# Kernel tuning notes

Measured on AMD Instinct MI355X. Metric: run time of the kernel, lower is better.

The kernel has to match this reference:

```python
import jax, jax.numpy as jnp
import numpy as np

TOP_K = 10


def setup_inputs() -> dict:
    key = jax.random.key(0)
    x = jax.random.normal(key, (256, 1, 8192), dtype=jnp.float32)
    return {"x": x}


def reference(x):
    # x: [B, 1, S] real
    B, _, S = x.shape
    # torch.arange(1e-05, 1, 1/S) has exactly S elements for these S
    t = 1e-05 + jnp.arange(S, dtype=jnp.float32) / S            # [S]
    dft = jnp.fft.fft(x[:, 0, :], n=S, axis=-1, norm='ortho')   # [B, S] complex64
    mag = jnp.abs(dft)                                          # [B, S]
    top_idx = jnp.argsort(-mag, axis=-1)[:, :TOP_K]             # [B, k] int
    top_dft = jnp.take_along_axis(dft, top_idx, axis=1)         # [B, k] complex
    # complex exponential basis exp(-2j*pi*k*t), flipped along time
    phase = (-2j * jnp.pi) * (top_idx[:, :, None].astype(jnp.float32) * t[None, None, :])
    bs = jnp.exp(phase)[:, :, ::-1]                             # [B, k, S] complex
    bf = top_dft[:, :, None] * bs / jnp.sqrt(jnp.float32(S))    # [B, k, S]
    # F.pad((1,0), mode='replicate') then crop to S: shift right by 1, duplicate first col
    bf = jnp.concatenate([bf[:, :, :1], bf[:, :, :-1]], axis=-1)
    bf = bf[:, :, None, :]                                      # [B, k, 1, S]
    residual = x - jnp.sum(bf, axis=1)                          # [B, 1, S] complex
    return bf, residual
```

## Files before the change

kernel.cpp:

```cpp
#include <hip/hip_runtime.h>

#define NB    256
#define SLEN  8192
#define LOG2S 13
#define TOPK  10

#define RES_REAL   ((size_t)20971520)
#define FULL_ILV   ((size_t)46137344)

__device__ int   g_k [NB * TOPK];
__device__ float g_ar[NB * TOPK];
__device__ float g_ai[NB * TOPK];

__device__ __forceinline__ float sin_rev(float p) { return __builtin_amdgcn_sinf(p); }
__device__ __forceinline__ float cos_rev(float p) { return __builtin_amdgcn_cosf(p); }

__device__ __forceinline__ bool beats(float om, int oi, float wm, int wi) {
  return (om > wm * 1.0001f) || (om > wm * 0.9999f && oi < wi);
}

__device__ __forceinline__ int pad(int a) { return a + (a >> 5); }

typedef float f32x4 __attribute__((ext_vector_type(4)));
__device__ __forceinline__ void store_nt4(float* p, float a, float b, float c,
                                          float d) {
  f32x4 v = {a, b, c, d};
  __builtin_nontemporal_store(v, (f32x4*)p);
}

__device__ __forceinline__ void bfly(float& ur, float& ui, float& vr, float& vi,
                                     float p) {
  const float c = cos_rev(p);
  const float s = -sin_rev(p);
  const float dr = ur - vr, di = ui - vi;
  ur += vr; ui += vi;
  vr = dr * c - di * s;
  vi = dr * s + di * c;
}

template<int ST>
__device__ __forceinline__ void bfly3(float (&xr)[8], float (&xi)[8], int m) {
  const float inv8 = 1.f / (float)(ST * 8);
  const float inv4 = 1.f / (float)(ST * 4);
  const float inv2 = 1.f / (float)(ST * 2);
#pragma unroll
  for (int k = 0; k < 4; ++k)
    bfly(xr[k], xi[k], xr[k + 4], xi[k + 4], (float)(m + ST * k) * inv8);
#pragma unroll
  for (int g = 0; g < 2; ++g)
#pragma unroll
    for (int k0 = 0; k0 < 2; ++k0) {
      const int k = g * 4 + k0;
      bfly(xr[k], xi[k], xr[k + 2], xi[k + 2], (float)(m + ST * k0) * inv4);
    }
  const float p1 = (float)m * inv2;
#pragma unroll
  for (int k = 0; k < 8; k += 2)
    bfly(xr[k], xi[k], xr[k + 1], xi[k + 1], p1);
}

__global__ __launch_bounds__(1024)
void fft_topk(const float* __restrict__ x) {
  __shared__ float re[8448];
  __shared__ float im[8448];
  __shared__ float wred_m[2][16];
  __shared__ int   wred_i[2][16];

  const int b = blockIdx.x;
  const int t = threadIdx.x;
  const int lane = t & 63;
  const int wid  = t >> 6;
  const float* xb = x + (size_t)b * SLEN;

  float xr[8], xi[8];

#pragma unroll
  for (int k = 0; k < 8; ++k) { xr[k] = xb[t + (k << 10)]; xi[k] = 0.f; }
  bfly3<1024>(xr, xi, t);
#pragma unroll
  for (int k = 0; k < 8; ++k) {
    const int a = pad(t + (k << 10));
    re[a] = xr[k]; im[a] = xi[k];
  }
  __syncthreads();

  {
    const int m  = t & 127;
    const int i0 = m + ((t >> 7) << 10);
#pragma unroll
    for (int k = 0; k < 8; ++k) {
      const int a = pad(i0 + (k << 7));
      xr[k] = re[a]; xi[k] = im[a];
    }
    bfly3<128>(xr, xi, m);
#pragma unroll
    for (int k = 0; k < 8; ++k) {
      const int a = pad(i0 + (k << 7));
      re[a] = xr[k]; im[a] = xi[k];
    }
  }
  __syncthreads();

  {
    const int m  = t & 15;
    const int i0 = m + ((t >> 4) << 7);
#pragma unroll
    for (int k = 0; k < 8; ++k) {
      const int a = pad(i0 + (k << 4));
      xr[k] = re[a]; xi[k] = im[a];
    }
    bfly3<16>(xr, xi, m);
#pragma unroll
    for (int k = 0; k < 8; ++k) {
      const int a = pad(i0 + (k << 4));
      re[a] = xr[k]; im[a] = xi[k];
    }
  }
  __syncthreads();

  {
    const int m  = t & 1;
    const int i0 = m + ((t >> 1) << 4);
#pragma unroll
    for (int k = 0; k < 8; ++k) {
      const int a = pad(i0 + (k << 1));
      xr[k] = re[a]; xi[k] = im[a];
    }
    bfly3<2>(xr, xi, m);
#pragma unroll
    for (int k = 0; k < 8; ++k) {
      const int a = pad(i0 + (k << 1));
      re[a] = xr[k]; im[a] = xi[k];
    }
  }
  __syncthreads();

#pragma unroll
  for (int q = 0; q < 8; ++q) {
    const int a = pad((t << 3) + q);
    xr[q] = re[a]; xi[q] = im[a];
  }
#pragma unroll
  for (int q = 0; q < 8; q += 2) {
    const float ur = xr[q], ui = xi[q];
    const float vr = xr[q + 1], vi = xi[q + 1];
    xr[q] = ur + vr;     xi[q] = ui + vi;
    xr[q + 1] = ur - vr; xi[q + 1] = ui - vi;
  }

  float m2c[8];
#pragma unroll
  for (int q = 0; q < 8; ++q) m2c[q] = xr[q] * xr[q] + xi[q] * xi[q];

  const int rt = (int)(__brev((unsigned)t) >> 22);
  const int qord[8] = {0, 4, 2, 6, 1, 5, 3, 7};

  for (int sel = 0; sel < TOPK; ++sel) {
    float wm = -1.f; int wi = SLEN;
#pragma unroll
    for (int j = 0; j < 8; ++j) {
      const int q = qord[j];
      if (m2c[q] > wm * 1.0001f) { wm = m2c[q]; wi = rt + (j << 10); }
    }
    for (int off = 32; off > 0; off >>= 1) {
      const float om = __shfl_down(wm, off);
      const int   oi = __shfl_down(wi, off);
      if (beats(om, oi, wm, wi)) { wm = om; wi = oi; }
    }
    const int par = sel & 1;
    if (lane == 0) { wred_m[par][wid] = wm; wred_i[par][wid] = wi; }
    __syncthreads();
    float cm = -1.f; int ci = SLEN;
    if (lane < 16) { cm = wred_m[par][lane]; ci = wred_i[par][lane]; }
    for (int off = 8; off > 0; off >>= 1) {
      const float om = __shfl_down(cm, off);
      const int   oi = __shfl_down(ci, off);
      if (beats(om, oi, cm, ci)) { cm = om; ci = oi; }
    }
    wm = __shfl(cm, 0); wi = __shfl(ci, 0);
    const int p = (int)(__brev((unsigned)wi) >> 19);
    if ((p >> 3) == t) {
      const int q = p & 7;
      const float rr = xr[q] * (1.f / (float)SLEN);
      const float ii = xi[q] * (1.f / (float)SLEN);
      const float pr = -1e-5f * (float)wi;
      const float cp = cos_rev(pr), sp = sin_rev(pr);
      g_k [b * TOPK + sel] = wi;
      g_ar[b * TOPK + sel] = rr * cp - ii * sp;
      g_ai[b * TOPK + sel] = rr * sp + ii * cp;
      m2c[q] = 0.f;
    }
  }
}

__global__ __launch_bounds__(256, 4)
void gen(const float* __restrict__ x, float* __restrict__ out, size_t cap) {
  const int bs    = blockIdx.x;
  const int b     = bs >> 3;
  const int slice = bs & 7;
  const int t     = threadIdx.x;
  const int s0    = slice * 1024 + t * 4;
  const float* xb = x + (size_t)b * SLEN;

  int kj[TOPK]; float arj[TOPK], aij[TOPK];
#pragma unroll
  for (int j = 0; j < TOPK; ++j) {
    kj[j]  = g_k [b * TOPK + j];
    arj[j] = g_ar[b * TOPK + j];
    aij[j] = g_ai[b * TOPK + j];
  }

  if (cap < FULL_ILV) {
    const size_t bfbase = (size_t)b * TOPK * SLEN;
    const float4 xv = *(const float4*)(xb + s0);
    float acc0 = 0.f, acc1 = 0.f, acc2 = 0.f, acc3 = 0.f;
#pragma unroll
    for (int j = 0; j < TOPK; ++j) {
      const int k = kj[j];
      float br[4];
#pragma unroll
      for (int q = 0; q < 4; ++q) {
        const int s = s0 + q;
        const int m = (s == 0) ? 1 : s;
        const float p = (float)((k * m) & (SLEN - 1)) * (1.f / (float)SLEN);
        br[q] = arj[j] * cos_rev(p) - aij[j] * sin_rev(p);
      }
      acc0 += br[0]; acc1 += br[1]; acc2 += br[2]; acc3 += br[3];
      const size_t o = bfbase + (size_t)j * SLEN + s0;
      if (o + 4 <= cap)
        store_nt4(out + o, br[0], br[1], br[2], br[3]);
    }
    const size_t o = RES_REAL + (size_t)b * SLEN + s0;
    if (o + 4 <= cap)
      store_nt4(out + o, xv.x - acc0, xv.y - acc1, xv.z - acc2, xv.w - acc3);
  } else {
    const size_t bfbase = (size_t)b * TOPK * SLEN * 2;
    const float4 xv = *(const float4*)(xb + s0);
    float sr[4] = {0.f, 0.f, 0.f, 0.f}, si[4] = {0.f, 0.f, 0.f, 0.f};
#pragma unroll
    for (int j = 0; j < TOPK; ++j) {
      const int k = kj[j];
      float br[4], bi[4];
#pragma unroll
      for (int q = 0; q < 4; ++q) {
        const int s = s0 + q;
        const int m = (s == 0) ? 1 : s;
        const float p = (float)((k * m) & (SLEN - 1)) * (1.f / (float)SLEN);
        const float c = cos_rev(p), sv = sin_rev(p);
        br[q] = arj[j] * c - aij[j] * sv;
        bi[q] = arj[j] * sv + aij[j] * c;
        sr[q] += br[q]; si[q] += bi[q];
      }
      const size_t o = bfbase + ((size_t)j * SLEN + s0) * 2;
      if (o + 8 <= cap) {
        store_nt4(out + o,     br[0], bi[0], br[1], bi[1]);
        store_nt4(out + o + 4, br[2], bi[2], br[3], bi[3]);
      }
    }
    const size_t o = (size_t)41943040 + ((size_t)b * SLEN + s0) * 2;
    if (o + 8 <= cap) {
      store_nt4(out + o,     xv.x - sr[0], -si[0], xv.y - sr[1], -si[1]);
      store_nt4(out + o + 4, xv.z - sr[2], -si[2], xv.w - sr[3], -si[3]);
    }
  }
}

extern "C" void kernel_launch(void* const* d_in, const int* in_sizes, int n_in,
                              void* d_out, int out_size, void* d_ws, size_t ws_size,
                              hipStream_t stream) {
  const float* x = (const float*)d_in[0];
  float* out = (float*)d_out;
  fft_topk<<<NB, 1024, 0, stream>>>(x);
  gen<<<NB * 8, 256, 0, stream>>>(x, out, (size_t)out_size);
}
```

Baseline: 123.3 us.

## Fuse FFT top-k and basis generation into a single kernel

Merges the FFT/top-k kernel and the basis/residual generation kernel into one kernel per batch row. The selected frequencies and amplitudes now stay in shared memory instead of round-tripping through global buffers, and one kernel launch is dropped. Each of the 1024 threads now writes 8 outputs instead of 4. The FFT scratch is also switched from split re/im arrays to interleaved float2. The trade-off is that the generation phase now runs with only 256 blocks of 1024 threads instead of 2048 smaller blocks, which may reduce occupancy and overlap of the store-heavy phase.

After: 150.1 us. 1.22x slower.

```diff
diff --git a/kernel.cpp b/kernel.cpp
--- a/kernel.cpp
+++ b/kernel.cpp
@@ -7,10 +7,6 @@
 
 #define RES_REAL   ((size_t)20971520)
 #define FULL_ILV   ((size_t)46137344)
-
-__device__ int   g_k [NB * TOPK];
-__device__ float g_ar[NB * TOPK];
-__device__ float g_ai[NB * TOPK];
 
 __device__ __forceinline__ float sin_rev(float p) { return __builtin_amdgcn_sinf(p); }
 __device__ __forceinline__ float cos_rev(float p) { return __builtin_amdgcn_cosf(p); }
@@ -60,11 +56,13 @@
 }
 
 __global__ __launch_bounds__(1024)
-void fft_topk(const float* __restrict__ x) {
-  __shared__ float re[8448];
-  __shared__ float im[8448];
-  __shared__ float wred_m[2][16];
-  __shared__ int   wred_i[2][16];
+void fourier_all(const float* __restrict__ x, float* __restrict__ out,
+                 size_t cap) {
+  __shared__ float2 Z[8448];
+  __shared__ float  wred_m[2][16];
+  __shared__ int    wred_i[2][16];
+  __shared__ int    sk[TOPK];
+  __shared__ float  sar[TOPK], sai[TOPK];
 
   const int b = blockIdx.x;
   const int t = threadIdx.x;
@@ -78,10 +76,8 @@
   for (int k = 0; k < 8; ++k) { xr[k] = xb[t + (k << 10)]; xi[k] = 0.f; }
   bfly3<1024>(xr, xi, t);
 #pragma unroll
-  for (int k = 0; k < 8; ++k) {
-    const int a = pad(t + (k << 10));
-    re[a] = xr[k]; im[a] = xi[k];
-  }
+  for (int k = 0; k < 8; ++k)
+    Z[pad(t + (k << 10))] = make_float2(xr[k], xi[k]);
   __syncthreads();
 
   {
@@ -89,15 +85,13 @@
     const int i0 = m + ((t >> 7) << 10);
 #pragma unroll
     for (int k = 0; k < 8; ++k) {
-      const int a = pad(i0 + (k << 7));
-      xr[k] = re[a]; xi[k] = im[a];
+      const float2 v = Z[pad(i0 + (k << 7))];
+      xr[k] = v.x; xi[k] = v.y;
     }
     bfly3<128>(xr, xi, m);
 #pragma unroll
-    for (int k = 0; k < 8; ++k) {
-      const int a = pad(i0 + (k << 7));
-      re[a] = xr[k]; im[a] = xi[k];
-    }
+    for (int k = 0; k < 8; ++k)
+      Z[pad(i0 + (k << 7))] = make_float2(xr[k], xi[k]);
   }
   __syncthreads();
 
@@ -106,15 +100,13 @@
     const int i0 = m + ((t >> 4) << 7);
 #pragma unroll
     for (int k = 0; k < 8; ++k) {
-      const int a = pad(i0 + (k << 4));
-      xr[k] = re[a]; xi[k] = im[a];
+      const float2 v = Z[pad(i0 + (k << 4))];
+      xr[k] = v.x; xi[k] = v.y;
     }
     bfly3<16>(xr, xi, m);
 #pragma unroll
-    for (int k = 0; k < 8; ++k) {
-      const int a = pad(i0 + (k << 4));
-      re[a] = xr[k]; im[a] = xi[k];
-    }
+    for (int k = 0; k < 8; ++k)
+      Z[pad(i0 + (k << 4))] = make_float2(xr[k], xi[k]);
   }
   __syncthreads();
 
@@ -123,22 +115,20 @@
     const int i0 = m + ((t >> 1) << 4);
 #pragma unroll
     for (int k = 0; k < 8; ++k) {
-      const int a = pad(i0 + (k << 1));
-      xr[k] = re[a]; xi[k] = im[a];
+      const float2 v = Z[pad(i0 + (k << 1))];
+      xr[k] = v.x; xi[k] = v.y;
     }
     bfly3<2>(xr, xi, m);
 #pragma unroll
-    for (int k = 0; k < 8; ++k) {
-      const int a = pad(i0 + (k << 1));
-      re[a] = xr[k]; im[a] = xi[k];
-    }
+    for (int k = 0; k < 8; ++k)
+      Z[pad(i0 + (k << 1))] = make_float2(xr[k], xi[k]);
   }
   __syncthreads();
 
 #pragma unroll
   for (int q = 0; q < 8; ++q) {
-    const int a = pad((t << 3) + q);
-    xr[q] = re[a]; xi[q] = im[a];
+    const float2 v = Z[pad((t << 3) + q)];
+    xr[q] = v.x; xi[q] = v.y;
   }
 #pragma unroll
   for (int q = 0; q < 8; q += 2) {
@@ -185,64 +175,67 @@
       const float ii = xi[q] * (1.f / (float)SLEN);
       const float pr = -1e-5f * (float)wi;
       const float cp = cos_rev(pr), sp = sin_rev(pr);
-      g_k [b * TOPK + sel] = wi;
-      g_ar[b * TOPK + sel] = rr * cp - ii * sp;
-      g_ai[b * TOPK + sel] = rr * sp + ii * cp;
+      sk [sel] = wi;
+      sar[sel] = rr * cp - ii * sp;
+      sai[sel] = rr * sp + ii * cp;
       m2c[q] = 0.f;
     }
   }
-}
-
-__global__ __launch_bounds__(256, 4)
-void gen(const float* __restrict__ x, float* __restrict__ out, size_t cap) {
-  const int bs    = blockIdx.x;
-  const int b     = bs >> 3;
-  const int slice = bs & 7;
-  const int t     = threadIdx.x;
-  const int s0    = slice * 1024 + t * 4;
-  const float* xb = x + (size_t)b * SLEN;
+  __syncthreads();
 
   int kj[TOPK]; float arj[TOPK], aij[TOPK];
 #pragma unroll
   for (int j = 0; j < TOPK; ++j) {
-    kj[j]  = g_k [b * TOPK + j];
-    arj[j] = g_ar[b * TOPK + j];
-    aij[j] = g_ai[b * TOPK + j];
-  }
+    kj[j] = sk[j]; arj[j] = sar[j]; aij[j] = sai[j];
+  }
+  const int s0 = t << 3;
 
   if (cap < FULL_ILV) {
     const size_t bfbase = (size_t)b * TOPK * SLEN;
-    const float4 xv = *(const float4*)(xb + s0);
-    float acc0 = 0.f, acc1 = 0.f, acc2 = 0.f, acc3 = 0.f;
+    const float4 xv0 = *(const float4*)(xb + s0);
+    const float4 xv1 = *(const float4*)(xb + s0 + 4);
+    float acc[8];
+#pragma unroll
+    for (int q = 0; q < 8; ++q) acc[q] = 0.f;
 #pragma unroll
     for (int j = 0; j < TOPK; ++j) {
       const int k = kj[j];
-      float br[4];
-#pragma unroll
-      for (int q = 0; q < 4; ++q) {
+      float br[8];
+#pragma unroll
+      for (int q = 0; q < 8; ++q) {
         const int s = s0 + q;
         const int m = (s == 0) ? 1 : s;
         const float p = (float)((k * m) & (SLEN - 1)) * (1.f / (float)SLEN);
         br[q] = arj[j] * cos_rev(p) - aij[j] * sin_rev(p);
-      }
-      acc0 += br[0]; acc1 += br[1]; acc2 += br[2]; acc3 += br[3];
+        acc[q] += br[q];
+      }
       const size_t o = bfbase + (size_t)j * SLEN + s0;
-      if (o + 4 <= cap)
-        store_nt4(out + o, br[0], br[1], br[2], br[3]);
+      if (o + 8 <= cap) {
+        store_nt4(out + o,     br[0], br[1], br[2], br[3]);
+        store_nt4(out + o + 4, br[4], br[5], br[6], br[7]);
+      }
     }
     const size_t o = RES_REAL + (size_t)b * SLEN + s0;
-    if (o + 4 <= cap)
-      store_nt4(out + o, xv.x - acc0, xv.y - acc1, xv.z - acc2, xv.w - acc3);
+    if (o + 8 <= cap) {
+      store_nt4(out + o,     xv0.x - acc[0], xv0.y - acc[1], xv0.z - acc[2],
+                xv0.w - acc[3]);
+      store_nt4(out + o + 4, xv1.x - acc[4], xv1.y - acc[5], xv1.z - acc[6],
+                xv1.w - acc[7]);
+    }
   } else {
     const size_t bfbase = (size_t)b * TOPK * SLEN * 2;
-    const float4 xv = *(const float4*)(xb + s0);
-    float sr[4] = {0.f, 0.f, 0.f, 0.f}, si[4] = {0.f, 0.f, 0.f, 0.f};
+    const float4 xv0 = *(const float4*)(xb + s0);
+    const float4 xv1 = *(const float4*)(xb + s0 + 4);
+    const float xs[8] = {xv0.x, xv0.y, xv0.z, xv0.w, xv1.x, xv1.y, xv1.z, xv1.w};
+    float sr[8], si[8];
+#pragma unroll
+    for (int q = 0; q < 8; ++q) { sr[q] = 0.f; si[q] = 0.f; }
 #pragma unroll
     for (int j = 0; j < TOPK; ++j) {
       const int k = kj[j];
-      float br[4], bi[4];
-#pragma unroll
-      for (int q = 0; q < 4; ++q) {
+      float br[8], bi[8];
+#pragma unroll
+      for (int q = 0; q < 8; ++q) {
         const int s = s0 + q;
         const int m = (s == 0) ? 1 : s;
         const float p = (float)((k * m) & (SLEN - 1)) * (1.f / (float)SLEN);
@@ -252,15 +245,19 @@
         sr[q] += br[q]; si[q] += bi[q];
       }
       const size_t o = bfbase + ((size_t)j * SLEN + s0) * 2;
-      if (o + 8 <= cap) {
-        store_nt4(out + o,     br[0], bi[0], br[1], bi[1]);
-        store_nt4(out + o + 4, br[2], bi[2], br[3], bi[3]);
+      if (o + 16 <= cap) {
+        store_nt4(out + o,      br[0], bi[0], br[1], bi[1]);
+        store_nt4(out + o + 4,  br[2], bi[2], br[3], bi[3]);
+        store_nt4(out + o + 8,  br[4], bi[4], br[5], bi[5]);
+        store_nt4(out + o + 12, br[6], bi[6], br[7], bi[7]);
       }
     }
     const size_t o = (size_t)41943040 + ((size_t)b * SLEN + s0) * 2;
-    if (o + 8 <= cap) {
-      store_nt4(out + o,     xv.x - sr[0], -si[0], xv.y - sr[1], -si[1]);
-      store_nt4(out + o + 4, xv.z - sr[2], -si[2], xv.w - sr[3], -si[3]);
+    if (o + 16 <= cap) {
+      store_nt4(out + o,      xs[0] - sr[0], -si[0], xs[1] - sr[1], -si[1]);
+      store_nt4(out + o + 4,  xs[2] - sr[2], -si[2], xs[3] - sr[3], -si[3]);
+      store_nt4(out + o + 8,  xs[4] - sr[4], -si[4], xs[5] - sr[5], -si[5]);
+      store_nt4(out + o + 12, xs[6] - sr[6], -si[6], xs[7] - sr[7], -si[7]);
     }
   }
 }
@@ -270,6 +267,5 @@
                               hipStream_t stream) {
   const float* x = (const float*)d_in[0];
   float* out = (float*)d_out;
-  fft_topk<<<NB, 1024, 0, stream>>>(x);
-  gen<<<NB * 8, 256, 0, stream>>>(x, out, (size_t)out_size);
-}
+  fourier_all<<<NB, 1024, 0, stream>>>(x, out, (size_t)out_size);
+}
```
